# Performance work log

Hardware: AMD Instinct MI355X
Metric: run time of the kernel (lower is better)

The kernel has to match this reference:

```python
import jax, jax.numpy as jnp
import numpy as np

B, N, D = 32, 16384, 256
SAMPLE = 256                      # nsample = samplepoint
NPOINT = int(np.ceil(N / SAMPLE))
DEPTH, HEADS = 2, 4
MLP_H = 512                       # int(256 * 2.0)
NUM_CLASSES = 40
EPS = 1e-5


def bn(x, g, b, m, v):
    # eval-mode BatchNorm over the last (channel) axis
    return (x - m) * (g * jax.lax.rsqrt(v + EPS)) + b


def ln(x, g, b):
    mu = jnp.mean(x, -1, keepdims=True)
    var = jnp.var(x, -1, keepdims=True)
    return (x - mu) * jax.lax.rsqrt(var + EPS) * g + b


def gather(p, i):
    # p: [B, N, ...], i: [B, ...] int -> p[b, i[b]]
    return jax.vmap(lambda a, idx: a[idx])(p, i)


def fps(xyz, npoint):
    # farthest point sampling, deterministic start at index 0. xyz: [B,N,3]
    Bb, Nn, _ = xyz.shape
    def step(carry, _):
        dist, far = carry
        c = gather(xyz, far)[:, None, :]                  # [B,1,3]
        dist = jnp.minimum(dist, jnp.sum((xyz - c) ** 2, -1))
        return (dist, jnp.argmax(dist, -1)), far
    init = (jnp.full((Bb, Nn), 1e10, xyz.dtype), jnp.zeros((Bb,), jnp.int32))
    _, idx = jax.lax.scan(step, init, None, length=npoint)
    return idx.T                                          # [B, npoint]


def reference(x, conv1_w, bn1_g, bn1_b, bn1_m, bn1_v,
              conv2_w, bn2_g, bn2_b, bn2_m, bn2_v,
              local_w, lbn_g, lbn_b, lbn_m, lbn_v, cls_token,
              ln1_g, ln1_b, qkv_w, proj_w, proj_b,
              ln2_g, ln2_b, fc1_w, fc1_b, fc2_w, fc2_b,
              norm_g, norm_b,
              h0_w, h0bn_g, h0bn_b, h0bn_m, h0bn_v,
              h1_w, h1bn_g, h1bn_b, h1bn_m, h1bn_v,
              se1_w, sebn_g, sebn_b, sebn_m, sebn_v, se2_w,
              h2_w, h2_b):
    xyz = jax.lax.stop_gradient(jnp.transpose(x, (0, 2, 1)))  # detach -> [B,N,3]
    h = jnp.einsum('bcn,dc->bnd', x, conv1_w)
    h = jax.nn.leaky_relu(bn(h, bn1_g, bn1_b, bn1_m, bn1_v), 0.2)
    h = jnp.einsum('bnd,ed->bne', h, conv2_w)
    points = jax.nn.leaky_relu(bn(h, bn2_g, bn2_b, bn2_m, bn2_v), 0.2)  # [B,N,64]

    # sample_and_group: FPS centers + kNN groups, feature = cat(local - center, center)
    fps_idx = fps(xyz, NPOINT)                                 # [B,S]
    new_xyz = gather(xyz, fps_idx)                             # [B,S,3]
    d2 = jnp.sum((new_xyz[:, :, None, :] - xyz[:, None, :, :]) ** 2, -1)  # [B,S,N]
    _, knn_idx = jax.lax.top_k(-d2, SAMPLE)                    # [B,S,K]
    grouped = gather(points, knn_idx)                          # [B,S,K,64]
    center = gather(points, fps_idx)                           # [B,S,64]
    feat = jnp.concatenate([grouped - center[:, :, None, :],
                            jnp.broadcast_to(center[:, :, None, :], grouped.shape)], -1)  # [B,S,K,128]

    # Local_op: 1x1 conv + BN + ReLU + max over group
    g = jax.nn.relu(bn(jnp.einsum('bskd,ed->bske', feat, local_w), lbn_g, lbn_b, lbn_m, lbn_v))
    tok = jnp.max(g, axis=2)                                   # [B,S,256]

    cls = jnp.broadcast_to(jnp.transpose(cls_token, (0, 2, 1)), (tok.shape[0], 1, D))
    t = jnp.concatenate([cls, tok], axis=1)                    # [B,S+1,D]

    hd = D // HEADS
    scale = hd ** -0.5
    for i in range(DEPTH):
        y = ln(t, ln1_g[i], ln1_b[i])
        qkv = jnp.einsum('btd,ed->bte', y, qkv_w[i]).reshape(t.shape[0], -1, 3, HEADS, hd)
        q, k, v = qkv[:, :, 0], qkv[:, :, 1], qkv[:, :, 2]     # [B,T,H,hd]
        a = jax.nn.softmax(jnp.einsum('bthd,bshd->bhts', q, k) * scale, axis=-1)
        o = jnp.einsum('bhts,bshd->bthd', a, v).reshape(t.shape[0], -1, D)
        t = t + jnp.einsum('btd,ed->bte', o, proj_w[i]) + proj_b[i]
        y = ln(t, ln2_g[i], ln2_b[i])
        y = jax.nn.gelu(jnp.einsum('btd,hd->bth', y, fc1_w[i]) + fc1_b[i], approximate=False)
        t = t + jnp.einsum('bth,dh->btd', y, fc2_w[i]) + fc2_b[i]
    t = ln(t, norm_g, norm_b)

    h = jax.nn.relu(bn(jnp.einsum('btd,ed->bte', t, h0_w), h0bn_g, h0bn_b, h0bn_m, h0bn_v))  # [B,T,1024]
    pooled = jnp.concatenate([jnp.max(h, axis=1), jnp.mean(h, axis=1)], axis=-1)  # [B,2048]
    z = jax.nn.relu(bn(pooled @ h1_w.T, h1bn_g, h1bn_b, h1bn_m, h1bn_v))          # [B,512]
    s = bn(z @ se1_w.T, sebn_g, sebn_b, sebn_m, sebn_v)
    s = jax.nn.sigmoid(jax.nn.leaky_relu(s, 0.2) @ se2_w.T)
    z = z * s                                                  # SE gate; dropout = identity (eval)
    return z @ h2_w.T + h2_b                                   # [B, NUM_CLASSES]


def setup_inputs():
    key = jax.random.key(0)
    ki = iter(jax.random.split(key, 64))
    r = lambda shape, s=0.05: jax.random.normal(next(ki), shape, jnp.float32) * s
    ones = lambda *s: jnp.ones(s, jnp.float32)
    zeros = lambda *s: jnp.zeros(s, jnp.float32)
    inp = dict(
        x=jax.random.normal(next(ki), (B, 3, N), jnp.float32),
        conv1_w=r((64, 3), 0.3), bn1_g=ones(64), bn1_b=zeros(64), bn1_m=zeros(64), bn1_v=ones(64),
        conv2_w=r((64, 64), 0.1), bn2_g=ones(64), bn2_b=zeros(64), bn2_m=zeros(64), bn2_v=ones(64),
        local_w=r((D, 128), 0.08), lbn_g=ones(D), lbn_b=zeros(D), lbn_m=zeros(D), lbn_v=ones(D),
        cls_token=r((1, D, 1), 0.02),
        ln1_g=ones(DEPTH, D), ln1_b=zeros(DEPTH, D),
        qkv_w=r((DEPTH, 3 * D, D)), proj_w=r((DEPTH, D, D)), proj_b=zeros(DEPTH, D),
        ln2_g=ones(DEPTH, D), ln2_b=zeros(DEPTH, D),
        fc1_w=r((DEPTH, MLP_H, D)), fc1_b=zeros(DEPTH, MLP_H),
        fc2_w=r((DEPTH, D, MLP_H)), fc2_b=zeros(DEPTH, D),
        norm_g=ones(D), norm_b=zeros(D),
        h0_w=r((1024, D)), h0bn_g=ones(1024), h0bn_b=zeros(1024), h0bn_m=zeros(1024), h0bn_v=ones(1024),
        h1_w=r((512, 2048), 0.02), h1bn_g=ones(512), h1bn_b=zeros(512), h1bn_m=zeros(512), h1bn_v=ones(512),
        se1_w=r((64, 512)), sebn_g=ones(64), sebn_b=zeros(64), sebn_m=zeros(64), sebn_v=ones(64),
        se2_w=r((512, 64)),
        h2_w=r((NUM_CLASSES, 512)), h2_b=zeros(NUM_CLASSES),
    )
    return inp
```

## Files before the change

kernel.cpp:

```cpp
#include <hip/hip_runtime.h>
#include <math.h>

#define B_   32
#define N_   16384
#define DD   256
#define NP_  64
#define SMP  256
#define TT   65
#define MT   2080
#define EPSF 1e-5f

typedef __attribute__((ext_vector_type(8))) short short8;
typedef __attribute__((ext_vector_type(4))) float floatx4;

__device__ __forceinline__ unsigned short f2bf(float f) {
  unsigned u = __float_as_uint(f);
  u += 0x7fffu + ((u >> 16) & 1u);
  return (unsigned short)(u >> 16);
}
__device__ __forceinline__ float bf2f(unsigned short h) {
  return __uint_as_float(((unsigned)h) << 16);
}
__device__ __forceinline__ int mn64(int a) { return a > 64 ? 64 : a; }

__device__ __forceinline__ float dist2p(const float* xb, int n, float cx, float cy, float cz) {
  float dx = xb[n] - cx, dy = xb[N_ + n] - cy, dz = xb[2 * N_ + n] - cz;
  return __fadd_rn(__fadd_rn(__fmul_rn(dx, dx), __fmul_rn(dy, dy)), __fmul_rn(dz, dz));
}

__global__ void prep_kernel(
    const float* bn1_g, const float* bn1_b, const float* bn1_m, const float* bn1_v,
    const float* bn2_g, const float* bn2_b, const float* bn2_m, const float* bn2_v,
    const float* lbn_g, const float* lbn_b, const float* lbn_m, const float* lbn_v,
    const float* h0_g, const float* h0_b, const float* h0_m, const float* h0_v,
    const float* h1_g, const float* h1_b, const float* h1_m, const float* h1_v,
    const float* se_g, const float* se_b, const float* se_m, const float* se_v,
    const float* cls, float* bnp, float* t)
{
  int tid = threadIdx.x;
#define BNPREP(CNT, G, Bp, Mp, Vp, So, Oo)                                   \
  for (int i = tid; i < (CNT); i += 256) {                                   \
    float S = G[i] * (1.0f / sqrtf(Vp[i] + EPSF));                           \
    bnp[(So) + i] = S; bnp[(Oo) + i] = Bp[i] - Mp[i] * S;                    \
  }
  BNPREP(64, bn1_g, bn1_b, bn1_m, bn1_v, 0, 64)
  BNPREP(64, bn2_g, bn2_b, bn2_m, bn2_v, 128, 192)
  BNPREP(256, lbn_g, lbn_b, lbn_m, lbn_v, 256, 512)
  BNPREP(1024, h0_g, h0_b, h0_m, h0_v, 768, 1792)
  BNPREP(512, h1_g, h1_b, h1_m, h1_v, 2816, 3328)
  BNPREP(64, se_g, se_b, se_m, se_v, 3840, 3904)
#undef BNPREP
  for (int i = tid; i < B_ * DD; i += 256)
    t[(size_t)(i >> 8) * TT * DD + (i & 255)] = cls[i & 255];
}

__global__ __launch_bounds__(256) void wprep_kernel(
    const float* __restrict__ qkv_w, const float* __restrict__ proj_w,
    const float* __restrict__ fc1_w, const float* __restrict__ fc2_w,
    const float* __restrict__ h0_w, unsigned short* __restrict__ wbf)
{
  int idx = blockIdx.x * 256 + threadIdx.x;
  if (idx >= 1310720) return;
  float v;
  if (idx < 393216) v = qkv_w[idx];
  else if (idx < 524288) v = proj_w[idx - 393216];
  else if (idx < 786432) v = fc1_w[idx - 524288];
  else if (idx < 1048576) v = fc2_w[idx - 786432];
  else v = h0_w[idx - 1048576];
  wbf[idx] = f2bf(v);
}

__global__ __launch_bounds__(256) void conv_kernel(
    const float* __restrict__ x, const float* __restrict__ conv1_w,
    const float* __restrict__ conv2_w, const float* __restrict__ bnp,
    unsigned short* __restrict__ points)
{
  __shared__ __align__(16) unsigned short Abuf[256 * 64];
  __shared__ __align__(16) unsigned short Bbuf[64 * 64];
  __shared__ float w1s[192];
  __shared__ float s1[64], o1[64], s2[64], o2[64];
  int tid = threadIdx.x;
  int blk = blockIdx.x;
  int b = blk >> 6;
  int n0 = (blk & 63) << 8;

  if (tid < 192) w1s[tid] = conv1_w[tid];
  if (tid >= 192) {
    int i = tid - 192;
    s1[i] = bnp[i]; o1[i] = bnp[64 + i];
    s2[i] = bnp[128 + i]; o2[i] = bnp[192 + i];
  }
  if (tid < 64) {
    const float* wr = conv2_w + tid * 64;
    char* Bb = (char*)Bbuf;
    for (int j = 0; j < 8; ++j) {
      union { unsigned short us[8]; int4 v4; } pk;
#pragma unroll
      for (int q = 0; q < 8; ++q) pk.us[q] = f2bf(wr[j * 8 + q]);
      *(int4*)(Bb + tid * 128 + ((j * 16) ^ ((tid & 7) << 4))) = pk.v4;
    }
  }
  __syncthreads();

  const float* xb = x + (size_t)b * 3 * N_;
  int n = n0 + tid;
  float x0 = xb[n], x1 = xb[N_ + n], x2 = xb[2 * N_ + n];
  char* Ab = (char*)Abuf;
  for (int j = 0; j < 8; ++j) {
    union { unsigned short us[8]; int4 v4; } pk;
#pragma unroll
    for (int q = 0; q < 8; ++q) {
      int jj = j * 8 + q;
      float h = x0 * w1s[jj * 3 + 0] + x1 * w1s[jj * 3 + 1] + x2 * w1s[jj * 3 + 2];
      h = h * s1[jj] + o1[jj];
      h = (h >= 0.f) ? h : 0.2f * h;
      pk.us[q] = f2bf(h);
    }
    *(int4*)(Ab + tid * 128 + ((j * 16) ^ ((tid & 7) << 4))) = pk.v4;
  }
  __syncthreads();

  int wv_ = tid >> 6, lane = tid & 63;
  int l15 = lane & 15, lg = lane >> 4;
  short8 bfrag[4][2];
#pragma unroll
  for (int nt = 0; nt < 4; ++nt)
#pragma unroll
    for (int ks = 0; ks < 2; ++ks) {
      int col = nt * 16 + l15;
      bfrag[nt][ks] = *(short8*)((char*)Bbuf + col * 128 + (((ks * 64) + (lg << 4)) ^ ((col & 7) << 4)));
    }
#pragma unroll
  for (int mt = 0; mt < 4; ++mt) {
    int row = wv_ * 64 + mt * 16 + l15;
    short8 af[2];
#pragma unroll
    for (int ks = 0; ks < 2; ++ks)
      af[ks] = *(short8*)((char*)Abuf + row * 128 + (((ks * 64) + (lg << 4)) ^ ((row & 7) << 4)));
#pragma unroll
    for (int nt = 0; nt < 4; ++nt) {
      floatx4 acc = {0.f, 0.f, 0.f, 0.f};
      acc = __builtin_amdgcn_mfma_f32_16x16x32_bf16(af[0], bfrag[nt][0], acc, 0, 0, 0);
      acc = __builtin_amdgcn_mfma_f32_16x16x32_bf16(af[1], bfrag[nt][1], acc, 0, 0, 0);
      int e = nt * 16 + l15;
      float S = s2[e], O = o2[e];
#pragma unroll
      for (int r = 0; r < 4; ++r) {
        float v = acc[r] * S + O;
        v = (v >= 0.f) ? v : 0.2f * v;
        int orow = wv_ * 64 + mt * 16 + lg * 4 + r;
        Abuf[orow * 64 + e] = f2bf(v);
      }
    }
  }
  __syncthreads();
  int4* d4 = (int4*)(points + (size_t)(b * N_ + n0) * 64);
  int4* s4v = (int4*)Abuf;
  for (int i = tid; i < 2048; i += 256) d4[i] = s4v[i];
}

__global__ __launch_bounds__(1024) void fps_kernel(
    const float* __restrict__ x, int* __restrict__ fps_idx, float* __restrict__ new_xyz)
{
  int b = blockIdx.x, tid = threadIdx.x;
  int lane = tid & 63;
  const float* xb = x + (size_t)b * 3 * N_;
  float px[16], py[16], pz[16], dist[16];
#pragma unroll
  for (int i = 0; i < 16; ++i) {
    int n = tid + (i << 10);
    px[i] = xb[n]; py[i] = xb[N_ + n]; pz[i] = xb[2 * N_ + n];
    dist[i] = 1e10f;
  }
  __shared__ unsigned long long key[3];
  if (tid < 3) key[tid] = 0ull;
  __syncthreads();
  int far = 0;
  for (int it = 0; it < NP_; ++it) {
    float cx = xb[far], cy = xb[N_ + far], cz = xb[2 * N_ + far];
    if (tid == 0) {
      fps_idx[b * NP_ + it] = far;
      float* nx = new_xyz + (b * NP_ + it) * 3;
      nx[0] = cx; nx[1] = cy; nx[2] = cz;
    }
    float bv = -1.f;
    int bi = 0;
#pragma unroll
    for (int i = 0; i < 16; ++i) {
      float dx = px[i] - cx, dy = py[i] - cy, dz = pz[i] - cz;
      float d = __fadd_rn(__fadd_rn(__fmul_rn(dx, dx), __fmul_rn(dy, dy)), __fmul_rn(dz, dz));
      float nd = fminf(dist[i], d);
      dist[i] = nd;
      if (nd > bv) { bv = nd; bi = tid + (i << 10); }
    }
    unsigned long long k = ((unsigned long long)__float_as_uint(bv) << 32) | (unsigned)(~bi);
#pragma unroll
    for (int off = 1; off < 64; off <<= 1) {
      unsigned long long o = __shfl_xor(k, off);
      k = (o > k) ? o : k;
    }
    int slot = it % 3;
    if (lane == 0) atomicMax(&key[slot], k);
    if (tid == 0) key[(it + 1) % 3] = 0ull;
    __syncthreads();
    far = (int)(~((unsigned)(key[slot] & 0xFFFFFFFFull))) & (N_ - 1);
  }
}

__global__ __launch_bounds__(1024) void knn_kernel(
    const float* __restrict__ x, const float* __restrict__ new_xyz,
    int* __restrict__ knn_idx)
{
  __shared__ __align__(16) unsigned hist[256];
  __shared__ unsigned c_less, c_eq;
  __shared__ int eqlist[128];
  int tid = threadIdx.x;
  int lane = tid & 63;
  int bs = blockIdx.x;
  int b = bs >> 6;
  const float* xb = x + (size_t)b * 3 * N_;
  float cx = new_xyz[bs * 3 + 0], cy = new_xyz[bs * 3 + 1], cz = new_xyz[bs * 3 + 2];
  unsigned du[16];
#pragma unroll
  for (int i = 0; i < 16; ++i)
    du[i] = __float_as_uint(dist2p(xb, tid + (i << 10), cx, cy, cz));
  if (tid == 0) { c_less = 0; c_eq = 0; }
  unsigned prefix = 0, pmask = 0, kneed = SMP;
  for (int pass = 0; pass < 4; ++pass) {
    int shift = 24 - 8 * pass;
    if (tid < 64) ((int4*)hist)[tid] = int4{0, 0, 0, 0};
    __syncthreads();
    if (pass == 0) {
#pragma unroll
      for (int i = 0; i < 16; ++i) {
        int bkt = (int)(du[i] >> 24);
        unsigned long long m = ~0ull;
        while (m) {
          int leader = __ffsll((long long)m) - 1;
          int lb = __shfl(bkt, leader);
          unsigned long long same = __ballot(bkt == lb);
          if (lane == leader) atomicAdd(&hist[lb], (unsigned)__popcll(same));
          m &= ~same;
        }
      }
    } else {
#pragma unroll
      for (int i = 0; i < 16; ++i) {
        unsigned u = du[i];
        if ((u & pmask) == prefix) atomicAdd(&hist[(u >> shift) & 255u], 1u);
      }
    }
    __syncthreads();
    unsigned h0 = hist[lane * 4], h1v = hist[lane * 4 + 1];
    unsigned h2v = hist[lane * 4 + 2], h3v = hist[lane * 4 + 3];
    unsigned s4 = h0 + h1v + h2v + h3v;
    unsigned cum = s4;
#pragma unroll
    for (int off = 1; off < 64; off <<= 1) {
      unsigned o = __shfl_up(cum, off);
      if (lane >= off) cum += o;
    }
    unsigned excl = cum - s4;
    bool hit = (cum >= kneed && excl < kneed);
    unsigned selbkt = 0, sub = 0;
    if (hit) {
      unsigned kk = kneed - excl;
      unsigned dsel;
      if (kk <= h0) { dsel = 0; sub = kk; }
      else if (kk <= h0 + h1v) { dsel = 1; sub = kk - h0; }
      else if (kk <= h0 + h1v + h2v) { dsel = 2; sub = kk - h0 - h1v; }
      else { dsel = 3; sub = kk - h0 - h1v - h2v; }
      selbkt = lane * 4 + dsel;
    }
    unsigned long long hm = __ballot(hit);
    int hl = __ffsll((long long)hm) - 1;
    selbkt = __shfl(selbkt, hl);
    sub = __shfl(sub, hl);
    prefix |= selbkt << shift;
    pmask |= 0xFFu << shift;
    kneed = sub;
    __syncthreads();
  }
  int* outp = knn_idx + (size_t)bs * SMP;
#pragma unroll
  for (int i = 0; i < 16; ++i) {
    unsigned u = du[i];
    int n = tid + (i << 10);
    bool pl = (u < prefix);
    unsigned long long m = __ballot(pl);
    if (m) {
      int leader = __ffsll((long long)m) - 1;
      int base = 0;
      if (lane == leader) base = (int)atomicAdd(&c_less, (unsigned)__popcll(m));
      base = __shfl(base, leader);
      if (pl) outp[base + __popcll(m & ((1ull << lane) - 1))] = n;
    }
    bool pe = (u == prefix);
    m = __ballot(pe);
    if (m) {
      int leader = __ffsll((long long)m) - 1;
      int base = 0;
      if (lane == leader) base = (int)atomicAdd(&c_eq, (unsigned)__popcll(m));
      base = __shfl(base, leader);
      if (pe) {
        unsigned p = (unsigned)base + (unsigned)__popcll(m & ((1ull << lane) - 1));
        if (p < 128) eqlist[p] = n;
      }
    }
  }
  __syncthreads();
  unsigned nl = c_less;
  unsigned ne = c_eq < 128u ? c_eq : 128u;
  for (int tI = tid; tI < (int)ne; tI += 1024) {
    int nt = eqlist[tI];
    unsigned rank = 0;
    for (unsigned j = 0; j < ne; ++j) rank += (eqlist[j] < nt) ? 1u : 0u;
    if (rank < kneed) outp[nl + rank] = nt;
  }
}

__global__ __launch_bounds__(256) void local_kernel(
    const unsigned short* __restrict__ points, const float* __restrict__ local_w,
    const int* __restrict__ knn_idx, const int* __restrict__ fps_idx,
    const float* __restrict__ bnp, float* __restrict__ t)
{
  __shared__ __align__(16) unsigned short Abuf[128 * 64];
  __shared__ __align__(16) unsigned short Bbuf[256 * 64];
  __shared__ float Sarr[256], Oarr[256], cl[64];
  __shared__ int kn[256];
  int tid = threadIdx.x;
  int bs = blockIdx.x;
  int b = bs >> 6, s = bs & 63;
  kn[tid] = knn_idx[(size_t)bs * SMP + tid] & (N_ - 1);
  if (tid < 64) {
    int nc = fps_idx[bs];
    cl[tid] = bf2f(points[((size_t)b * N_ + nc) * 64 + tid]);
  }
  __syncthreads();
  {
    int e = tid;
    const float* wr = local_w + e * 128;
    float beta = 0.f;
    char* Bb = (char*)Bbuf;
    for (int j = 0; j < 8; ++j) {
      union { unsigned short us[8]; int4 v4; } pk;
#pragma unroll
      for (int q = 0; q < 8; ++q) {
        int d = j * 8 + q;
        float w1v = wr[d], w2v = wr[64 + d];
        beta += cl[d] * (w2v - w1v);
        pk.us[q] = f2bf(w1v);
      }
      *(int4*)(Bb + e * 128 + ((j * 16) ^ ((e & 7) << 4))) = pk.v4;
    }
    float S = bnp[256 + e];
    Sarr[e] = S;
    Oarr[e] = bnp[512 + e] + beta * S;
  }
  {
    int row = tid >> 1, part = tid & 1;
    int n = kn[row];
    const int4* src = (const int4*)(points + ((size_t)b * N_ + n) * 64);
    char* Ab = (char*)Abuf;
    for (int j = part * 4; j < part * 4 + 4; ++j)
      *(int4*)(Ab + row * 128 + ((j * 16) ^ ((row & 7) << 4))) = src[j];
  }
  __syncthreads();
  int wv_ = tid >> 6, lane = tid & 63, l15 = lane & 15, lg = lane >> 4;
  float cm[4] = {0.f, 0.f, 0.f, 0.f};
  short8 bfrag[4][2];
#pragma unroll
  for (int nt = 0; nt < 4; ++nt)
#pragma unroll
    for (int ks = 0; ks < 2; ++ks) {
      int col = wv_ * 64 + nt * 16 + l15;
      bfrag[nt][ks] = *(short8*)((char*)Bbuf + col * 128 + (((ks * 64) + (lg << 4)) ^ ((col & 7) << 4)));
    }
  for (int half = 0; half < 2; ++half) {
    if (half == 1) {
      __syncthreads();
      int row = tid >> 1, part = tid & 1;
      int n = kn[128 + row];
      const int4* src = (const int4*)(points + ((size_t)b * N_ + n) * 64);
      char* Ab = (char*)Abuf;
      for (int j = part * 4; j < part * 4 + 4; ++j)
        *(int4*)(Ab + row * 128 + ((j * 16) ^ ((row & 7) << 4))) = src[j];
      __syncthreads();
    }
#pragma unroll
    for (int mt = 0; mt < 8; ++mt) {
      int row = mt * 16 + l15;
      short8 af[2];
#pragma unroll
      for (int ks = 0; ks < 2; ++ks)
        af[ks] = *(short8*)((char*)Abuf + row * 128 + (((ks * 64) + (lg << 4)) ^ ((row & 7) << 4)));
#pragma unroll
      for (int nt = 0; nt < 4; ++nt) {
        floatx4 acc = {0.f, 0.f, 0.f, 0.f};
        acc = __builtin_amdgcn_mfma_f32_16x16x32_bf16(af[0], bfrag[nt][0], acc, 0, 0, 0);
        acc = __builtin_amdgcn_mfma_f32_16x16x32_bf16(af[1], bfrag[nt][1], acc, 0, 0, 0);
        int e = wv_ * 64 + nt * 16 + l15;
        float S = Sarr[e], O = Oarr[e];
        float vm = 0.f;
#pragma unroll
        for (int r = 0; r < 4; ++r) {
          float v = fmaxf(acc[r] * S + O, 0.f);
          vm = fmaxf(vm, v);
        }
        cm[nt] = fmaxf(cm[nt], vm);
      }
    }
  }
#pragma unroll
  for (int nt = 0; nt < 4; ++nt) {
    float v = cm[nt];
    v = fmaxf(v, __shfl_xor(v, 16));
    v = fmaxf(v, __shfl_xor(v, 32));
    if (lane < 16)
      t[(size_t)(b * TT + 1 + s) * DD + wv_ * 64 + nt * 16 + l15] = v;
  }
}

__global__ __launch_bounds__(256) void ln_kernel(
    const float* __restrict__ in, unsigned short* __restrict__ out,
    const float* __restrict__ g, const float* __restrict__ bb, int M)
{
  int row = blockIdx.x * 4 + (threadIdx.x >> 6);
  int lane = threadIdx.x & 63;
  if (row >= M) return;
  const float* xr = in + (size_t)row * DD;
  float4 v = *(const float4*)(xr + lane * 4);
  float sm = v.x + v.y + v.z + v.w;
#pragma unroll
  for (int off = 32; off; off >>= 1) sm += __shfl_xor(sm, off);
  float mu = sm * (1.f / DD);
  float d0 = v.x - mu, d1 = v.y - mu, d2 = v.z - mu, d3 = v.w - mu;
  float sq = d0 * d0 + d1 * d1 + d2 * d2 + d3 * d3;
#pragma unroll
  for (int off = 32; off; off >>= 1) sq += __shfl_xor(sq, off);
  float rs = 1.0f / sqrtf(sq * (1.f / DD) + EPSF);
  float4 gv = *(const float4*)(g + lane * 4);
  float4 bv = *(const float4*)(bb + lane * 4);
  unsigned short* orow = out + (size_t)row * DD + lane * 4;
  unsigned p0 = (unsigned)f2bf(d0 * rs * gv.x + bv.x) | ((unsigned)f2bf(d1 * rs * gv.y + bv.y) << 16);
  unsigned p1 = (unsigned)f2bf(d2 * rs * gv.z + bv.z) | ((unsigned)f2bf(d3 * rs * gv.w + bv.w) << 16);
  ((unsigned*)orow)[0] = p0;
  ((unsigned*)orow)[1] = p1;
}

__global__ __launch_bounds__(256) void bgemm_kernel(
    const unsigned short* __restrict__ A, const unsigned short* __restrict__ W,
    float* __restrict__ C, unsigned short* __restrict__ Cb, int M, int N, int K,
    const float* __restrict__ bias, const float* __restrict__ res,
    const float* __restrict__ bnS, const float* __restrict__ bnO, int act)
{
  __shared__ __align__(16) unsigned short As[64 * 64];
  __shared__ __align__(16) unsigned short Bs[64 * 64];
  int tid = threadIdx.x;
  int m0 = blockIdx.y << 6, n0 = blockIdx.x << 6;
  int lr = tid >> 2;
  int c0 = (tid & 3) << 4;
  int wv = tid >> 6, lane = tid & 63, l15 = lane & 15, lg = lane >> 4;
  int wr = (wv >> 1) << 5, wc = (wv & 1) << 5;
  int swzA = (lr & 7) << 4;
  floatx4 acc[2][2];
#pragma unroll
  for (int i = 0; i < 2; ++i)
#pragma unroll
    for (int j = 0; j < 2; ++j) acc[i][j] = floatx4{0.f, 0.f, 0.f, 0.f};

  char* Ab = (char*)As;
  char* Bb = (char*)Bs;
  int gm_s = m0 + lr;

  for (int k0 = 0; k0 < K; k0 += 64) {
    int4 a0v, a1v;
    if (gm_s < M) {
      const int4* p = (const int4*)(A + (size_t)gm_s * K + k0 + c0);
      a0v = p[0]; a1v = p[1];
    } else {
      a0v = int4{0, 0, 0, 0}; a1v = int4{0, 0, 0, 0};
    }
    *(int4*)(Ab + lr * 128 + ((c0 * 2) ^ swzA)) = a0v;
    *(int4*)(Ab + lr * 128 + ((c0 * 2 + 16) ^ swzA)) = a1v;
    {
      const int4* q = (const int4*)(W + (size_t)(n0 + lr) * K + k0 + c0);
      *(int4*)(Bb + lr * 128 + ((c0 * 2) ^ swzA)) = q[0];
      *(int4*)(Bb + lr * 128 + ((c0 * 2 + 16) ^ swzA)) = q[1];
    }
    __syncthreads();
    short8 af[2][2], bf[2][2];
#pragma unroll
    for (int mt = 0; mt < 2; ++mt) {
      int row = wr + mt * 16 + l15;
#pragma unroll
      for (int ks = 0; ks < 2; ++ks)
        af[mt][ks] = *(short8*)(Ab + row * 128 + (((ks * 64) + (lg << 4)) ^ ((row & 7) << 4)));
    }
#pragma unroll
    for (int nt = 0; nt < 2; ++nt) {
      int col = wc + nt * 16 + l15;
#pragma unroll
      for (int ks = 0; ks < 2; ++ks)
        bf[nt][ks] = *(short8*)(Bb + col * 128 + (((ks * 64) + (lg << 4)) ^ ((col & 7) << 4)));
    }
#pragma unroll
    for (int mt = 0; mt < 2; ++mt)
#pragma unroll
      for (int nt = 0; nt < 2; ++nt) {
        acc[mt][nt] = __builtin_amdgcn_mfma_f32_16x16x32_bf16(af[mt][0], bf[nt][0], acc[mt][nt], 0, 0, 0);
        acc[mt][nt] = __builtin_amdgcn_mfma_f32_16x16x32_bf16(af[mt][1], bf[nt][1], acc[mt][nt], 0, 0, 0);
      }
    __syncthreads();
  }
#pragma unroll
  for (int mt = 0; mt < 2; ++mt) {
#pragma unroll
    for (int r = 0; r < 4; ++r) {
      int gm = m0 + wr + mt * 16 + lg * 4 + r;
      if (gm >= M) continue;
#pragma unroll
      for (int nt = 0; nt < 2; ++nt) {
        int gn = n0 + wc + nt * 16 + l15;
        float v = acc[mt][nt][r];
        if (bias) v += bias[gn];
        if (res) v += res[(size_t)gm * N + gn];
        if (act == 1) v = 0.5f * v * (1.f + erff(v * 0.70710678118654752f));
        else if (act == 2) v = fmaxf(v * bnS[gn] + bnO[gn], 0.f);
        if (Cb) Cb[(size_t)gm * N + gn] = f2bf(v);
        else C[(size_t)gm * N + gn] = v;
      }
    }
  }
}

__global__ __launch_bounds__(256) void h1_kernel(
    const float* __restrict__ pooled, const float* __restrict__ h1_w,
    const float* __restrict__ bnS, const float* __restrict__ bnO,
    float* __restrict__ z)
{
  __shared__ __align__(16) float wrow[2048];
  int n = blockIdx.x;
  int tid = threadIdx.x;
  const float4* wsrc = (const float4*)(h1_w + (size_t)n * 2048);
  ((float4*)wrow)[tid] = wsrc[tid];
  ((float4*)wrow)[tid + 256] = wsrc[tid + 256];
  __syncthreads();
  int wv = tid >> 6, lane = tid & 63;
  int m0 = wv * 8;
  int kb = lane * 32;
  float acc[8] = {0.f, 0.f, 0.f, 0.f, 0.f, 0.f, 0.f, 0.f};
  for (int j = 0; j < 8; ++j) {
    float4 w4 = *(float4*)&wrow[kb + j * 4];
#pragma unroll
    for (int r = 0; r < 8; ++r) {
      float4 pv = *(const float4*)(pooled + (size_t)(m0 + r) * 2048 + kb + j * 4);
      acc[r] += pv.x * w4.x + pv.y * w4.y + pv.z * w4.z + pv.w * w4.w;
    }
  }
#pragma unroll
  for (int r = 0; r < 8; ++r) {
#pragma unroll
    for (int off = 32; off; off >>= 1) acc[r] += __shfl_xor(acc[r], off);
  }
  if (lane == 0) {
    float S = bnS[n], O = bnO[n];
#pragma unroll
    for (int r = 0; r < 8; ++r)
      z[(size_t)(m0 + r) * 512 + n] = fmaxf(acc[r] * S + O, 0.f);
  }
}

__global__ __launch_bounds__(256) void attn_kernel(
    const float* __restrict__ qkv, unsigned short* __restrict__ o)
{
  __shared__ float uni[TT][72];
  __shared__ float ks[TT][72];
  __shared__ float vs[TT][72];
  int tid = threadIdx.x;
  int b = blockIdx.x >> 2, h = blockIdx.x & 3;
  const float* base = qkv + (size_t)b * TT * 768 + h * 64;
  for (int i = tid; i < TT * 64; i += 256) {
    int t_ = i >> 6, d = i & 63;
    const float* p = base + (size_t)t_ * 768 + d;
    uni[t_][d] = p[0];
    ks[t_][d] = p[256];
    vs[t_][d] = p[512];
  }
  __syncthreads();
  float stile[2][16];
#pragma unroll
  for (int pi = 0; pi < 2; ++pi) {
    int p = tid + pi * 256;
    if (p >= 289) continue;
    int ti = (p / 17) * 4, tj = (p % 17) * 4;
    float a[16];
#pragma unroll
    for (int q = 0; q < 16; ++q) a[q] = 0.f;
    for (int kk = 0; kk < 64; kk += 4) {
      float4 qv[4], kv[4];
#pragma unroll
      for (int i2 = 0; i2 < 4; ++i2) qv[i2] = *(float4*)&uni[mn64(ti + i2)][kk];
#pragma unroll
      for (int j2 = 0; j2 < 4; ++j2) kv[j2] = *(float4*)&ks[mn64(tj + j2)][kk];
#pragma unroll
      for (int i2 = 0; i2 < 4; ++i2)
#pragma unroll
        for (int j2 = 0; j2 < 4; ++j2)
          a[i2 * 4 + j2] += qv[i2].x * kv[j2].x + qv[i2].y * kv[j2].y +
                            qv[i2].z * kv[j2].z + qv[i2].w * kv[j2].w;
    }
#pragma unroll
    for (int q = 0; q < 16; ++q) stile[pi][q] = a[q];
  }
  __syncthreads();
#pragma unroll
  for (int pi = 0; pi < 2; ++pi) {
    int p = tid + pi * 256;
    if (p >= 289) continue;
    int ti = (p / 17) * 4, tj = (p % 17) * 4;
#pragma unroll
    for (int i2 = 0; i2 < 4; ++i2)
#pragma unroll
      for (int j2 = 0; j2 < 4; ++j2)
        uni[mn64(ti + i2)][mn64(tj + j2)] = stile[pi][i2 * 4 + j2] * 0.125f;
  }
  __syncthreads();
  int wv_ = tid >> 6, lane = tid & 63;
  for (int r = wv_; r < TT; r += 4) {
    float v0 = uni[r][lane];
    float v1 = (lane == 0) ? uni[r][64] : -1e30f;
    float mx = fmaxf(v0, v1);
#pragma unroll
    for (int off = 32; off; off >>= 1) mx = fmaxf(mx, __shfl_xor(mx, off));
    float e0 = expf(v0 - mx);
    float e1 = (lane == 0) ? expf(v1 - mx) : 0.f;
    float ssum = e0 + e1;
#pragma unroll
    for (int off = 32; off; off >>= 1) ssum += __shfl_xor(ssum, off);
    float inv = 1.f / ssum;
    uni[r][lane] = e0 * inv;
    if (lane == 0) uni[r][64] = e1 * inv;
  }
  __syncthreads();
#pragma unroll
  for (int pi = 0; pi < 2; ++pi) {
    int p = tid + pi * 256;
    if (p >= 272) continue;
    int ti = (p >> 4) * 4, dj = (p & 15) * 4;
    float a[16];
#pragma unroll
    for (int q = 0; q < 16; ++q) a[q] = 0.f;
    for (int ts = 0; ts < TT; ++ts) {
      float4 vv = *(float4*)&vs[ts][dj];
#pragma unroll
      for (int i2 = 0; i2 < 4; ++i2) {
        float av = uni[mn64(ti + i2)][ts];
        a[i2 * 4 + 0] += av * vv.x;
        a[i2 * 4 + 1] += av * vv.y;
        a[i2 * 4 + 2] += av * vv.z;
        a[i2 * 4 + 3] += av * vv.w;
      }
    }
#pragma unroll
    for (int i2 = 0; i2 < 4; ++i2) {
      int r = ti + i2;
      if (r <= 64) {
        unsigned short* op = o + ((size_t)b * TT + r) * DD + h * 64 + dj;
        ((unsigned*)op)[0] = (unsigned)f2bf(a[i2 * 4 + 0]) | ((unsigned)f2bf(a[i2 * 4 + 1]) << 16);
        ((unsigned*)op)[1] = (unsigned)f2bf(a[i2 * 4 + 2]) | ((unsigned)f2bf(a[i2 * 4 + 3]) << 16);
      }
    }
  }
}

__global__ __launch_bounds__(256) void pool_kernel(const float* __restrict__ hb, float* __restrict__ pooled)
{
  int b = blockIdx.x, tid = threadIdx.x;
  for (int e = tid; e < 1024; e += 256) {
    const float* p = hb + (size_t)b * TT * 1024 + e;
    float mx = -1e30f, sm = 0.f;
    for (int t_ = 0; t_ < TT; ++t_) {
      float v = p[(size_t)t_ * 1024];
      mx = fmaxf(mx, v);
      sm += v;
    }
    pooled[b * 2048 + e] = mx;
    pooled[b * 2048 + 1024 + e] = sm / 65.0f;
  }
}

__global__ __launch_bounds__(256) void se_out_kernel(
    const float* __restrict__ z, const float* __restrict__ se1_w,
    const float* __restrict__ bnp, const float* __restrict__ se2_w,
    const float* __restrict__ h2_w, const float* __restrict__ h2_b,
    float* __restrict__ outp)
{
  __shared__ float zs[512], s1[64], z2[512];
  int b = blockIdx.x, tid = threadIdx.x;
  zs[tid] = z[b * 512 + tid];
  zs[256 + tid] = z[b * 512 + 256 + tid];
  __syncthreads();
  if (tid < 64) {
    const float* wr = se1_w + tid * 512;
    float acc = 0.f;
    for (int j = 0; j < 512; ++j) acc = fmaf(zs[j], wr[j], acc);
    float v = acc * bnp[3840 + tid] + bnp[3904 + tid];
    s1[tid] = (v >= 0.f) ? v : 0.2f * v;
  }
  __syncthreads();
  for (int cc = tid; cc < 512; cc += 256) {
    const float* wr = se2_w + cc * 64;
    float acc = 0.f;
    for (int j = 0; j < 64; ++j) acc = fmaf(s1[j], wr[j], acc);
    float sg = 1.f / (1.f + expf(-acc));
    z2[cc] = zs[cc] * sg;
  }
  __syncthreads();
  if (tid < 40) {
    const float* wr = h2_w + tid * 512;
    float acc = 0.f;
    for (int j = 0; j < 512; ++j) acc = fmaf(z2[j], wr[j], acc);
    outp[b * 40 + tid] = acc + h2_b[tid];
  }
}

extern "C" void kernel_launch(void* const* d_in, const int* in_sizes, int n_in,
                              void* d_out, int out_size, void* d_ws, size_t ws_size,
                              hipStream_t stream)
{
  (void)in_sizes; (void)n_in; (void)out_size; (void)ws_size;
  const float* x       = (const float*)d_in[0];
  const float* conv1_w = (const float*)d_in[1];
  const float* bn1_g   = (const float*)d_in[2];
  const float* bn1_b   = (const float*)d_in[3];
  const float* bn1_m   = (const float*)d_in[4];
  const float* bn1_v   = (const float*)d_in[5];
  const float* conv2_w = (const float*)d_in[6];
  const float* bn2_g   = (const float*)d_in[7];
  const float* bn2_b   = (const float*)d_in[8];
  const float* bn2_m   = (const float*)d_in[9];
  const float* bn2_v   = (const float*)d_in[10];
  const float* local_w = (const float*)d_in[11];
  const float* lbn_g   = (const float*)d_in[12];
  const float* lbn_b   = (const float*)d_in[13];
  const float* lbn_m   = (const float*)d_in[14];
  const float* lbn_v   = (const float*)d_in[15];
  const float* cls     = (const float*)d_in[16];
  const float* ln1_g   = (const float*)d_in[17];
  const float* ln1_b   = (const float*)d_in[18];
  const float* qkv_w   = (const float*)d_in[19];
  const float* proj_w  = (const float*)d_in[20];
  const float* proj_b  = (const float*)d_in[21];
  const float* ln2_g   = (const float*)d_in[22];
  const float* ln2_b   = (const float*)d_in[23];
  const float* fc1_w   = (const float*)d_in[24];
  const float* fc1_b   = (const float*)d_in[25];
  const float* fc2_w   = (const float*)d_in[26];
  const float* fc2_b   = (const float*)d_in[27];
  const float* norm_g  = (const float*)d_in[28];
  const float* norm_b  = (const float*)d_in[29];
  const float* h0_w    = (const float*)d_in[30];
  const float* h1_w    = (const float*)d_in[35];
  const float* se1_w   = (const float*)d_in[40];
  const float* se2_w   = (const float*)d_in[45];
  const float* h2_w    = (const float*)d_in[46];
  const float* h2_b    = (const float*)d_in[47];
  const float* h0bn_g  = (const float*)d_in[31];
  const float* h0bn_b  = (const float*)d_in[32];
  const float* h0bn_m  = (const float*)d_in[33];
  const float* h0bn_v  = (const float*)d_in[34];
  const float* h1bn_g  = (const float*)d_in[36];
  const float* h1bn_b  = (const float*)d_in[37];
  const float* h1bn_m  = (const float*)d_in[38];
  const float* h1bn_v  = (const float*)d_in[39];
  const float* sebn_g  = (const float*)d_in[41];
  const float* sebn_b  = (const float*)d_in[42];
  const float* sebn_m  = (const float*)d_in[43];
  const float* sebn_v  = (const float*)d_in[44];

  char* ws = (char*)d_ws;
  unsigned short* points = (unsigned short*)ws;
  const size_t P = 67108864;
  int*   fpsidx = (int*)(ws + P);
  float* nxyz   = (float*)(ws + P + 8192);
  int*   knn    = (int*)(ws + P + 32768);
  float* bnp    = (float*)(ws + P + 2129920);
  float* tbuf   = (float*)(ws + P + 2146304);
  unsigned short* ybuf = (unsigned short*)(ws + 0);
  float* qkvbuf = (float*)(ws + 2129920);
  unsigned short* obuf = (unsigned short*)(ws + 8519680);
  unsigned short* hmlp = (unsigned short*)(ws + 10649600);
  float* hbuf   = (float*)(ws + 14909440);
  float* pooled = (float*)(ws + 23429120);
  float* zbuf   = (float*)(ws + 23691264);
  unsigned short* wbf = (unsigned short*)(ws + 31457280);
  unsigned short* qkvw_bf = wbf;
  unsigned short* projw_bf = wbf + 393216;
  unsigned short* fc1w_bf = wbf + 524288;
  unsigned short* fc2w_bf = wbf + 786432;
  unsigned short* h0w_bf  = wbf + 1048576;

  prep_kernel<<<1, 256, 0, stream>>>(
      bn1_g, bn1_b, bn1_m, bn1_v, bn2_g, bn2_b, bn2_m, bn2_v,
      lbn_g, lbn_b, lbn_m, lbn_v, h0bn_g, h0bn_b, h0bn_m, h0bn_v,
      h1bn_g, h1bn_b, h1bn_m, h1bn_v, sebn_g, sebn_b, sebn_m, sebn_v,
      cls, bnp, tbuf);
  conv_kernel<<<2048, 256, 0, stream>>>(x, conv1_w, conv2_w, bnp, points);
  fps_kernel<<<32, 1024, 0, stream>>>(x, fpsidx, nxyz);
  knn_kernel<<<2048, 1024, 0, stream>>>(x, nxyz, knn);
  local_kernel<<<2048, 256, 0, stream>>>(points, local_w, knn, fpsidx, bnp, tbuf);
  wprep_kernel<<<5120, 256, 0, stream>>>(qkv_w, proj_w, fc1_w, fc2_w, h0_w, wbf);

  for (int i = 0; i < 2; ++i) {
    ln_kernel<<<520, 256, 0, stream>>>(tbuf, ybuf, ln1_g + i * 256, ln1_b + i * 256, MT);
    bgemm_kernel<<<dim3(12, 33), 256, 0, stream>>>(ybuf, qkvw_bf + (size_t)i * 196608, qkvbuf, nullptr,
                                                   MT, 768, 256, nullptr, nullptr, nullptr, nullptr, 0);
    attn_kernel<<<128, 256, 0, stream>>>(qkvbuf, obuf);
    bgemm_kernel<<<dim3(4, 33), 256, 0, stream>>>(obuf, projw_bf + (size_t)i * 65536, tbuf, nullptr,
                                                  MT, 256, 256, proj_b + i * 256, tbuf, nullptr, nullptr, 0);
    ln_kernel<<<520, 256, 0, stream>>>(tbuf, ybuf, ln2_g + i * 256, ln2_b + i * 256, MT);
    bgemm_kernel<<<dim3(8, 33), 256, 0, stream>>>(ybuf, fc1w_bf + (size_t)i * 131072, nullptr, hmlp,
                                                  MT, 512, 256, fc1_b + i * 512, nullptr, nullptr, nullptr, 1);
    bgemm_kernel<<<dim3(4, 33), 256, 0, stream>>>(hmlp, fc2w_bf + (size_t)i * 131072, tbuf, nullptr,
                                                  MT, 256, 512, fc2_b + i * 256, tbuf, nullptr, nullptr, 0);
  }

  ln_kernel<<<520, 256, 0, stream>>>(tbuf, ybuf, norm_g, norm_b, MT);
  bgemm_kernel<<<dim3(16, 33), 256, 0, stream>>>(ybuf, h0w_bf, hbuf, nullptr, MT, 1024, 256,
                                                 nullptr, nullptr, bnp + 768, bnp + 1792, 2);
  pool_kernel<<<32, 256, 0, stream>>>(hbuf, pooled);
  h1_kernel<<<512, 256, 0, stream>>>(pooled, h1_w, bnp + 2816, bnp + 3328, zbuf);
  se_out_kernel<<<32, 256, 0, stream>>>(zbuf, se1_w, bnp, se2_w, h2_w, h2_b, (float*)d_out);
}
```

Baseline: 569.6 us.

## Restructure kNN radix select to 256 threads with per-wave histograms

The kNN selection kernel now runs 256 threads per block, each holding 64 distances in registers instead of 16, with per-wave private histograms summed at scan time. The pass-0 ballot-based aggregation is replaced by plain shared atomics. Output compaction switches from per-iteration ballot/atomic to a per-thread count, a wave prefix scan and one atomic per wave, with sequential writes. This cuts block-wide sync width and atomic contention, at the cost of higher register pressure (64 live values) and less coalesced output stores.

```diff
diff --git a/kernel.cpp b/kernel.cpp
--- a/kernel.cpp
+++ b/kernel.cpp
@@ -207,52 +207,39 @@
   }
 }
 
-__global__ __launch_bounds__(1024) void knn_kernel(
+__global__ __launch_bounds__(256, 4) void knn_kernel(
     const float* __restrict__ x, const float* __restrict__ new_xyz,
     int* __restrict__ knn_idx)
 {
-  __shared__ __align__(16) unsigned hist[256];
+  __shared__ __align__(16) unsigned whist[4][256];
   __shared__ unsigned c_less, c_eq;
   __shared__ int eqlist[128];
   int tid = threadIdx.x;
-  int lane = tid & 63;
+  int lane = tid & 63, wv = tid >> 6;
   int bs = blockIdx.x;
   int b = bs >> 6;
   const float* xb = x + (size_t)b * 3 * N_;
   float cx = new_xyz[bs * 3 + 0], cy = new_xyz[bs * 3 + 1], cz = new_xyz[bs * 3 + 2];
-  unsigned du[16];
-#pragma unroll
-  for (int i = 0; i < 16; ++i)
-    du[i] = __float_as_uint(dist2p(xb, tid + (i << 10), cx, cy, cz));
+  unsigned du[64];
+#pragma unroll
+  for (int i = 0; i < 64; ++i)
+    du[i] = __float_as_uint(dist2p(xb, tid + (i << 8), cx, cy, cz));
   if (tid == 0) { c_less = 0; c_eq = 0; }
   unsigned prefix = 0, pmask = 0, kneed = SMP;
   for (int pass = 0; pass < 4; ++pass) {
     int shift = 24 - 8 * pass;
-    if (tid < 64) ((int4*)hist)[tid] = int4{0, 0, 0, 0};
+    ((int4*)whist)[tid] = int4{0, 0, 0, 0};
     __syncthreads();
-    if (pass == 0) {
-#pragma unroll
-      for (int i = 0; i < 16; ++i) {
-        int bkt = (int)(du[i] >> 24);
-        unsigned long long m = ~0ull;
-        while (m) {
-          int leader = __ffsll((long long)m) - 1;
-          int lb = __shfl(bkt, leader);
-          unsigned long long same = __ballot(bkt == lb);
-          if (lane == leader) atomicAdd(&hist[lb], (unsigned)__popcll(same));
-          m &= ~same;
-        }
-      }
-    } else {
-#pragma unroll
-      for (int i = 0; i < 16; ++i) {
-        unsigned u = du[i];
-        if ((u & pmask) == prefix) atomicAdd(&hist[(u >> shift) & 255u], 1u);
-      }
+#pragma unroll
+    for (int i = 0; i < 64; ++i) {
+      unsigned u = du[i];
+      if ((u & pmask) == prefix) atomicAdd(&whist[wv][(u >> shift) & 255u], 1u);
     }
     __syncthreads();
-    unsigned h0 = hist[lane * 4], h1v = hist[lane * 4 + 1];
-    unsigned h2v = hist[lane * 4 + 2], h3v = hist[lane * 4 + 3];
+    unsigned h0 = whist[0][lane * 4 + 0] + whist[1][lane * 4 + 0] + whist[2][lane * 4 + 0] + whist[3][lane * 4 + 0];
+    unsigned h1v = whist[0][lane * 4 + 1] + whist[1][lane * 4 + 1] + whist[2][lane * 4 + 1] + whist[3][lane * 4 + 1];
+    unsigned h2v = whist[0][lane * 4 + 2] + whist[1][lane * 4 + 2] + whist[2][lane * 4 + 2] + whist[3][lane * 4 + 2];
+    unsigned h3v = whist[0][lane * 4 + 3] + whist[1][lane * 4 + 3] + whist[2][lane * 4 + 3] + whist[3][lane * 4 + 3];
     unsigned s4 = h0 + h1v + h2v + h3v;
     unsigned cum = s4;
 #pragma unroll
@@ -281,37 +268,40 @@
     kneed = sub;
     __syncthreads();
   }
+  int cl = 0, ce = 0;
+#pragma unroll
+  for (int i = 0; i < 64; ++i) {
+    cl += (du[i] < prefix) ? 1 : 0;
+    ce += (du[i] == prefix) ? 1 : 0;
+  }
+  int cls = cl, ces = ce;
+#pragma unroll
+  for (int off = 1; off < 64; off <<= 1) {
+    int t1 = __shfl_up(cls, off);
+    int t2 = __shfl_up(ces, off);
+    if (lane >= off) { cls += t1; ces += t2; }
+  }
+  int excl_l = cls - cl, excl_e = ces - ce;
+  unsigned bl = 0, be = 0;
+  if (lane == 63) {
+    bl = atomicAdd(&c_less, (unsigned)cls);
+    be = atomicAdd(&c_eq, (unsigned)ces);
+  }
+  bl = __shfl(bl, 63);
+  be = __shfl(be, 63);
   int* outp = knn_idx + (size_t)bs * SMP;
-#pragma unroll
-  for (int i = 0; i < 16; ++i) {
+  unsigned po = bl + excl_l, pe = be + excl_e;
+#pragma unroll
+  for (int i = 0; i < 64; ++i) {
     unsigned u = du[i];
-    int n = tid + (i << 10);
-    bool pl = (u < prefix);
-    unsigned long long m = __ballot(pl);
-    if (m) {
-      int leader = __ffsll((long long)m) - 1;
-      int base = 0;
-      if (lane == leader) base = (int)atomicAdd(&c_less, (unsigned)__popcll(m));
-      base = __shfl(base, leader);
-      if (pl) outp[base + __popcll(m & ((1ull << lane) - 1))] = n;
-    }
-    bool pe = (u == prefix);
-    m = __ballot(pe);
-    if (m) {
-      int leader = __ffsll((long long)m) - 1;
-      int base = 0;
-      if (lane == leader) base = (int)atomicAdd(&c_eq, (unsigned)__popcll(m));
-      base = __shfl(base, leader);
-      if (pe) {
-        unsigned p = (unsigned)base + (unsigned)__popcll(m & ((1ull << lane) - 1));
-        if (p < 128) eqlist[p] = n;
-      }
-    }
+    int n = tid + (i << 8);
+    if (u < prefix) outp[po++] = n;
+    else if (u == prefix) { if (pe < 128u) eqlist[pe] = n; pe++; }
   }
   __syncthreads();
   unsigned nl = c_less;
   unsigned ne = c_eq < 128u ? c_eq : 128u;
-  for (int tI = tid; tI < (int)ne; tI += 1024) {
+  for (int tI = tid; tI < (int)ne; tI += 256) {
     int nt = eqlist[tI];
     unsigned rank = 0;
     for (unsigned j = 0; j < ne; ++j) rank += (eqlist[j] < nt) ? 1u : 0u;
@@ -808,7 +798,7 @@
       cls, bnp, tbuf);
   conv_kernel<<<2048, 256, 0, stream>>>(x, conv1_w, conv2_w, bnp, points);
   fps_kernel<<<32, 1024, 0, stream>>>(x, fpsidx, nxyz);
-  knn_kernel<<<2048, 1024, 0, stream>>>(x, nxyz, knn);
+  knn_kernel<<<2048, 256, 0, stream>>>(x, nxyz, knn);
   local_kernel<<<2048, 256, 0, stream>>>(points, local_w, knn, fpsidx, bnp, tbuf);
   wprep_kernel<<<5120, 256, 0, stream>>>(qkv_w, proj_w, fc1_w, fc2_w, h0_w, wbf);
 
```

Result: slower. 673.6 us (+18.3%).
